# Optimization experiments

Hardware: AMD Instinct MI355X
Metric: run time of the kernel (lower is better)

## Reference

```python
import jax, jax.numpy as jnp
import numpy as np

N = 4096   # in_features
M = 4096   # out_features
RANK, FT_RANK = 128, 64
Q_SCALE, R_SCALE, L_SCALE, GLOBAL_SCALE = 0.9, 1.05, 1.1, 1.0


def fwht(x):
    """Normalized fast Walsh-Hadamard transform over last dim (power of 2).
    Matches matmul_hadU/hadUt for power-of-2 sizes (H symmetric, 1/sqrt(n))."""
    B, n = x.shape
    y, h = x, 1
    while h < n:
        y = y.reshape(B, n // (2 * h), 2, h)
        a, b = y[:, :, 0, :], y[:, :, 1, :]
        y = jnp.stack((a + b, a - b), axis=2)
        h *= 2
    return y.reshape(B, n) * (1.0 / np.sqrt(n)).astype(np.float32)


def dequant(grid, idxs, scale, n_cols):
    # E8P dequant: gather 8-dim lattice vectors, reshape to [rows, n_cols].
    return grid[idxs].reshape(idxs.shape[0], n_cols) * jnp.float32(scale)


def setup_inputs() -> dict:
    key = jax.random.key(0)
    ks = jax.random.split(key, 9)
    return {
        "x": jax.random.normal(ks[0], (4, 2048, N), jnp.float32),
        "SU": jnp.sign(jax.random.normal(ks[1], (N,), jnp.float32)),
        "SV": jnp.sign(jax.random.normal(ks[2], (M,), jnp.float32)),
        "grid": jax.random.normal(ks[3], (65536, 8), jnp.float32) * 0.05,
        "L_ft": jax.random.normal(ks[4], (M, FT_RANK), jnp.float32) * 0.05,
        "R_ft": jax.random.normal(ks[5], (FT_RANK, N), jnp.float32) * 0.05,
        "Q_idxs": jax.random.randint(ks[6], (M, N // 8), 0, 65536, jnp.int32),
        "R_idxs": jax.random.randint(ks[7], (RANK - FT_RANK, N // 8), 0, 65536, jnp.int32),
        "L_idxs": jax.random.randint(ks[8], (RANK - FT_RANK, M // 8), 0, 65536, jnp.int32),
    }


def reference(x, SU, SV, grid, L_ft, R_ft, Q_idxs, R_idxs, L_idxs):
    shape = x.shape
    xf = x.reshape(-1, N) * SU            # [T, n]
    xh = fwht(xf)                          # left randomized Hadamard (hadUt)
    # Q path (x/32 then *scale*32 cancels; applied via scale on W).
    W_q = dequant(grid, Q_idxs, Q_SCALE, N)          # [m, n]
    out = xh @ W_q.T                                  # [T, m]
    # Quantized low-rank path: xR = x @ W_R^T; out += xR @ W_L (transposed L).
    W_r = dequant(grid, R_idxs, R_SCALE, N)           # [r, n]
    W_l = dequant(grid, L_idxs, L_SCALE, M)           # [r, m]
    xR = xh @ W_r.T                                   # [T, r]
    out = out + xR @ W_l                              # [T, m]
    # Fine-tunable LoRA path.
    out = out + (xh @ R_ft.T) @ L_ft.T                # [T, m]
    out = fwht(out)                                   # right Hadamard (hadU)
    out = out * SV * jnp.float32(GLOBAL_SCALE)
    return out.reshape(shape[:-1] + (M,))
```

## Files before the change

kernel.cpp:

```cpp
#include <hip/hip_runtime.h>
#include <stdint.h>
#include <stddef.h>


typedef __attribute__((ext_vector_type(8))) __bf16 bf16x8;
typedef __attribute__((ext_vector_type(4))) float f32x4;

#define DEVFN static __device__ __forceinline__

typedef const __attribute__((address_space(1))) void* as1cvp;
typedef __attribute__((address_space(3))) void* as3vp;

DEVFN void async_g2l16(const void* g, void* l) {
  __builtin_amdgcn_global_load_lds((as1cvp)g, (as3vp)l, 16, 0, 0);
}

DEVFN void fwht16(float* v) {
  #pragma unroll
  for (int h = 1; h < 16; h <<= 1) {
    #pragma unroll
    for (int i = 0; i < 16; ++i) {
      if ((i & h) == 0) {
        float a = v[i], b = v[i + h];
        v[i] = a + b;
        v[i + h] = a - b;
      }
    }
  }
}

DEVFN int padi(int i) { return i + (i >> 4) + (i >> 8); }

template<int MODE>
__global__ __launch_bounds__(256)
void fwht_rows(const float* in, const float* __restrict__ sgn,
               __bf16* __restrict__ outb, float* outf)
{
  __shared__ float s[4366];
  const int row = blockIdx.x;
  const int t = threadIdx.x;
  const float* src = in + (size_t)row * 4096;
  float v[16];

  #pragma unroll
  for (int j4 = 0; j4 < 4; ++j4) {
    f32x4 xv = *(const f32x4*)(src + t * 16 + j4 * 4);
    #pragma unroll
    for (int q = 0; q < 4; ++q) v[j4 * 4 + q] = xv[q];
  }
  if (MODE == 0) {
    #pragma unroll
    for (int j = 0; j < 16; ++j) v[j] *= sgn[t * 16 + j];
  }
  fwht16(v);
  {
    const int base = t * 17 + (t >> 4);
    #pragma unroll
    for (int j = 0; j < 16; ++j) s[base + j] = v[j];
  }
  __syncthreads();

  const int base2 = (t & 15) + ((t >> 4) << 8);
  #pragma unroll
  for (int i = 0; i < 16; ++i) v[i] = s[padi(base2 + (i << 4))];
  fwht16(v);
  #pragma unroll
  for (int i = 0; i < 16; ++i) s[padi(base2 + (i << 4))] = v[i];
  __syncthreads();

  #pragma unroll
  for (int i = 0; i < 16; ++i) v[i] = s[padi(t + (i << 8))];
  fwht16(v);

  if (MODE == 0) {
    #pragma unroll
    for (int i = 0; i < 16; ++i)
      outb[(size_t)row * 4096 + t + (i << 8)] = (__bf16)(v[i] * 0.015625f);
  } else {
    #pragma unroll
    for (int i = 0; i < 16; ++i) {
      int c = t + (i << 8);
      outf[(size_t)row * 4096 + c] = v[i] * 0.015625f * sgn[c];
    }
  }
}

__global__ __launch_bounds__(256)
void prep_uv(const float* __restrict__ grid8,
             const float* __restrict__ Lft, const float* __restrict__ Rft,
             const int* __restrict__ Lidx, const int* __restrict__ Ridx,
             __bf16* __restrict__ Ut, __bf16* __restrict__ Vt)
{
  int tid = blockIdx.x * 256 + threadIdx.x;
  const int half = 4096 * 128;
  bool isV = tid >= half;
  int e = isV ? tid - half : tid;
  int j = e >> 7;
  int r = e & 127;
  float v;
  if (!isV) {
    if (r < 64) v = 1.1f * grid8[(size_t)Lidx[r * 512 + (j >> 3)] * 8 + (j & 7)];
    else        v = Lft[(size_t)j * 64 + (r - 64)];
    Ut[e] = (__bf16)v;
  } else {
    if (r < 64) v = 1.05f * grid8[(size_t)Ridx[r * 512 + (j >> 3)] * 8 + (j & 7)];
    else        v = Rft[(size_t)(r - 64) * 4096 + j];
    Vt[e] = (__bf16)v;
  }
}

template<int K, int EPI>
__global__ __launch_bounds__(256)
void gemm_bt(const __bf16* __restrict__ A, const __bf16* __restrict__ B,
             float* __restrict__ Cf, __bf16* __restrict__ Cb,
             const int* __restrict__ Qidx, const float* __restrict__ grid8,
             int Nn, int nbx)
{
  __shared__ __bf16 sA[128 * 64];
  __shared__ __bf16 sB[128 * 64];

  const int nwg = gridDim.x;
  const int orig = blockIdx.x;
  const int cpx = nwg >> 3;
  const int wg = (orig & 7) * cpx + (orig >> 3);
  const int bm = wg / nbx, bn = wg % nbx;

  const int t = threadIdx.x;
  const int lane = t & 63;
  const int w = t >> 6;
  const int wr = w >> 1, wc = w & 1;

  const int aRow0 = bm * 128;
  const int bRow0 = bn * 128;

  f32x4 acc[4][4] = {};

  #pragma unroll 1
  for (int k0 = 0; k0 < K; k0 += 64) {
    #pragma unroll
    for (int i = 0; i < 4; ++i) {
      int u = i * 256 + t;
      int row = u >> 3, cs = u & 7;
      int c = cs ^ (row & 7);
      async_g2l16(A + (size_t)(aRow0 + row) * K + k0 + c * 8, &sA[u * 8]);
      async_g2l16(B + (size_t)(bRow0 + row) * K + k0 + c * 8, &sB[u * 8]);
    }
    asm volatile("s_waitcnt vmcnt(0)" ::: "memory");
    __syncthreads();

    bf16x8 a[4][2], b[4][2];
    #pragma unroll
    for (int m = 0; m < 4; ++m) {
      #pragma unroll
      for (int kk = 0; kk < 2; ++kk) {
        int c = kk * 4 + (lane >> 4);
        int rowA = wr * 64 + m * 16 + (lane & 15);
        int uA = rowA * 8 + (c ^ (rowA & 7));
        a[m][kk] = *(const bf16x8*)&sA[uA * 8];
        int rowB = wc * 64 + m * 16 + (lane & 15);
        int uB = rowB * 8 + (c ^ (rowB & 7));
        b[m][kk] = *(const bf16x8*)&sB[uB * 8];
      }
    }
    #pragma unroll
    for (int kk = 0; kk < 2; ++kk)
      #pragma unroll
      for (int m = 0; m < 4; ++m)
        #pragma unroll
        for (int n = 0; n < 4; ++n)
          acc[m][n] = __builtin_amdgcn_mfma_f32_16x16x32_bf16(
              a[m][kk], b[n][kk], acc[m][n], 0, 0, 0);
    __syncthreads();
  }

  #pragma unroll
  for (int m = 0; m < 4; ++m) {
    #pragma unroll
    for (int n = 0; n < 4; ++n) {
      int gr = aRow0 + wr * 64 + m * 16 + ((lane >> 4) << 2);
      int gc = bRow0 + wc * 64 + n * 16 + (lane & 15);
      #pragma unroll
      for (int q = 0; q < 4; ++q) {
        float v = acc[m][n][q];
        if constexpr (EPI == 0) {
          Cf[(size_t)(gr + q) * Nn + gc] = v;
        } else {
          int idx = Qidx[(size_t)(gr + q) * (Nn >> 3) + (gc >> 3)];
          v += 0.9f * grid8[(size_t)idx * 8 + (gc & 7)];
          Cb[(size_t)(gr + q) * Nn + gc] = (__bf16)v;
        }
      }
    }
  }
}

extern "C" void kernel_launch(void* const* d_in, const int* in_sizes, int n_in,
                              void* d_out, int out_size, void* d_ws, size_t ws_size,
                              hipStream_t stream) {
  const float* x    = (const float*)d_in[0];
  const float* SU   = (const float*)d_in[1];
  const float* SV   = (const float*)d_in[2];
  const float* grid = (const float*)d_in[3];
  const float* Lft  = (const float*)d_in[4];
  const float* Rft  = (const float*)d_in[5];
  const int*   Qidx = (const int*)d_in[6];
  const int*   Ridx = (const int*)d_in[7];
  const int*   Lidx = (const int*)d_in[8];
  float* out = (float*)d_out;

  char* ws = (char*)d_ws;
  __bf16* xh = (__bf16*)ws;
  __bf16* Wc = (__bf16*)(ws + ((size_t)64 << 20));
  __bf16* Ut = (__bf16*)(ws + ((size_t)96 << 20));
  __bf16* Vt = (__bf16*)(ws + ((size_t)97 << 20));

  prep_uv<<<4096, 256, 0, stream>>>(grid, Lft, Rft, Lidx, Ridx, Ut, Vt);
  fwht_rows<0><<<8192, 256, 0, stream>>>(x, SU, xh, nullptr);
  gemm_bt<128, 1><<<1024, 256, 0, stream>>>(Ut, Vt, nullptr, Wc, Qidx, grid, 4096, 32);
  gemm_bt<4096, 0><<<2048, 256, 0, stream>>>(xh, Wc, out, nullptr, nullptr, nullptr, 4096, 32);
  fwht_rows<1><<<8192, 256, 0, stream>>>(out, SV, nullptr, out);
}
```

Measured before the change: 663.2 us.

## Replace main GEMM with 256x256-tile, 4-stage pipelined kernel; vectorize FWHT I/O

The main 8192x4096x4096 GEMM moves from a 128x128 tile kernel, which loads and waits synchronously every k-step, to a 256x256 tile kernel with 512 threads. The new kernel uses a 4-deep LDS ring buffer prefetching three k-tiles ahead, partial vmcnt waits, and raised priority around the MFMA block. This aims to hide global load latency and cut redundant operand traffic, at the cost of a large LDS footprint and high register pressure per wave. The FWHT kernels also stage results through LDS so they can do contiguous vector stores, and they load the sign vectors with vector loads instead of strided scalar accesses.

```diff
diff --git a/kernel.cpp b/kernel.cpp
--- a/kernel.cpp
+++ b/kernel.cpp
@@ -39,25 +39,30 @@
   __shared__ float s[4366];
   const int row = blockIdx.x;
   const int t = threadIdx.x;
-  const float* src = in + (size_t)row * 4096;
+  const int base1 = t * 17 + (t >> 4);
   float v[16];
 
-  #pragma unroll
-  for (int j4 = 0; j4 < 4; ++j4) {
-    f32x4 xv = *(const f32x4*)(src + t * 16 + j4 * 4);
-    #pragma unroll
-    for (int q = 0; q < 4; ++q) v[j4 * 4 + q] = xv[q];
+  {
+    const float* src = in + (size_t)row * 4096 + t * 16;
+    #pragma unroll
+    for (int j4 = 0; j4 < 4; ++j4) {
+      f32x4 xv = *(const f32x4*)(src + j4 * 4);
+      #pragma unroll
+      for (int q = 0; q < 4; ++q) v[j4 * 4 + q] = xv[q];
+    }
   }
   if (MODE == 0) {
-    #pragma unroll
-    for (int j = 0; j < 16; ++j) v[j] *= sgn[t * 16 + j];
+    const f32x4* sg4 = (const f32x4*)(sgn + t * 16);
+    #pragma unroll
+    for (int j4 = 0; j4 < 4; ++j4) {
+      f32x4 sv = sg4[j4];
+      #pragma unroll
+      for (int q = 0; q < 4; ++q) v[j4 * 4 + q] *= sv[q];
+    }
   }
   fwht16(v);
-  {
-    const int base = t * 17 + (t >> 4);
-    #pragma unroll
-    for (int j = 0; j < 16; ++j) s[base + j] = v[j];
-  }
+  #pragma unroll
+  for (int j = 0; j < 16; ++j) s[base1 + j] = v[j];
   __syncthreads();
 
   const int base2 = (t & 15) + ((t >> 4) << 8);
@@ -71,16 +76,29 @@
   #pragma unroll
   for (int i = 0; i < 16; ++i) v[i] = s[padi(t + (i << 8))];
   fwht16(v);
+  #pragma unroll
+  for (int i = 0; i < 16; ++i) s[padi(t + (i << 8))] = v[i];
+  __syncthreads();
 
   if (MODE == 0) {
-    #pragma unroll
-    for (int i = 0; i < 16; ++i)
-      outb[(size_t)row * 4096 + t + (i << 8)] = (__bf16)(v[i] * 0.015625f);
+    bf16x8 o0, o1;
+    #pragma unroll
+    for (int j = 0; j < 8; ++j) o0[j] = (__bf16)(s[base1 + j] * 0.015625f);
+    #pragma unroll
+    for (int j = 0; j < 8; ++j) o1[j] = (__bf16)(s[base1 + 8 + j] * 0.015625f);
+    __bf16* dst = outb + (size_t)row * 4096 + t * 16;
+    *(bf16x8*)dst = o0;
+    *(bf16x8*)(dst + 8) = o1;
   } else {
-    #pragma unroll
-    for (int i = 0; i < 16; ++i) {
-      int c = t + (i << 8);
-      outf[(size_t)row * 4096 + c] = v[i] * 0.015625f * sgn[c];
+    const f32x4* sg4 = (const f32x4*)(sgn + t * 16);
+    float* dst = outf + (size_t)row * 4096 + t * 16;
+    #pragma unroll
+    for (int j4 = 0; j4 < 4; ++j4) {
+      f32x4 sv = sg4[j4];
+      f32x4 ov;
+      #pragma unroll
+      for (int q = 0; q < 4; ++q) ov[q] = s[base1 + j4 * 4 + q] * 0.015625f * sv[q];
+      *(f32x4*)(dst + j4 * 4) = ov;
     }
   }
 }
@@ -109,10 +127,10 @@
   }
 }
 
-template<int K, int EPI>
+template<int K>
 __global__ __launch_bounds__(256)
 void gemm_bt(const __bf16* __restrict__ A, const __bf16* __restrict__ B,
-             float* __restrict__ Cf, __bf16* __restrict__ Cb,
+             __bf16* __restrict__ Cb,
              const int* __restrict__ Qidx, const float* __restrict__ grid8,
              int Nn, int nbx)
 {
@@ -140,10 +158,10 @@
     #pragma unroll
     for (int i = 0; i < 4; ++i) {
       int u = i * 256 + t;
-      int row = u >> 3, cs = u & 7;
-      int c = cs ^ (row & 7);
-      async_g2l16(A + (size_t)(aRow0 + row) * K + k0 + c * 8, &sA[u * 8]);
-      async_g2l16(B + (size_t)(bRow0 + row) * K + k0 + c * 8, &sB[u * 8]);
+      int rowu = u >> 3, cs = u & 7;
+      int c = cs ^ (rowu & 7);
+      async_g2l16(A + (size_t)(aRow0 + rowu) * K + k0 + c * 8, &sA[u * 8]);
+      async_g2l16(B + (size_t)(bRow0 + rowu) * K + k0 + c * 8, &sB[u * 8]);
     }
     asm volatile("s_waitcnt vmcnt(0)" ::: "memory");
     __syncthreads();
@@ -182,14 +200,118 @@
       #pragma unroll
       for (int q = 0; q < 4; ++q) {
         float v = acc[m][n][q];
-        if constexpr (EPI == 0) {
-          Cf[(size_t)(gr + q) * Nn + gc] = v;
-        } else {
-          int idx = Qidx[(size_t)(gr + q) * (Nn >> 3) + (gc >> 3)];
-          v += 0.9f * grid8[(size_t)idx * 8 + (gc & 7)];
-          Cb[(size_t)(gr + q) * Nn + gc] = (__bf16)v;
-        }
+        int idx = Qidx[(size_t)(gr + q) * (Nn >> 3) + (gc >> 3)];
+        v += 0.9f * grid8[(size_t)idx * 8 + (gc & 7)];
+        Cb[(size_t)(gr + q) * Nn + gc] = (__bf16)v;
       }
+    }
+  }
+}
+
+template<int NT>
+__global__ __launch_bounds__(512, 2)
+void gemm256(const __bf16* __restrict__ A, const __bf16* __restrict__ B,
+             float* __restrict__ Cf, int Nn, int nbx)
+{
+  constexpr int K = NT * 32;
+  __shared__ __bf16 lds[4 * 2 * 8192];
+
+  const int nwg = gridDim.x;
+  const int orig = blockIdx.x;
+  const int cpx = nwg >> 3;
+  const int wg = (orig & 7) * cpx + (orig >> 3);
+  const int bm = wg / nbx, bn = wg % nbx;
+
+  const int tid = threadIdx.x;
+  const int lane = tid & 63;
+  const int wid = tid >> 6;
+  const int wm = wid >> 2;
+  const int wn = wid & 3;
+
+  const int aRow0 = bm * 256;
+  const int bRow0 = bn * 256;
+
+  auto stage = [&](int t) {
+    __bf16* dA = &lds[((t & 3) * 2 + 0) * 8192];
+    __bf16* dB = &lds[((t & 3) * 2 + 1) * 8192];
+    const __bf16* sAg = A + (size_t)aRow0 * K + t * 32;
+    const __bf16* sBg = B + (size_t)bRow0 * K + t * 32;
+    #pragma unroll
+    for (int i = 0; i < 2; ++i) {
+      int u = i * 512 + tid;
+      int prow = u >> 3, slot = u & 7;
+      int chunk = slot ^ (prow & 7);
+      int r = 2 * prow + (chunk >> 2);
+      int k8 = chunk & 3;
+      async_g2l16(sAg + (size_t)r * K + k8 * 8, dA + u * 8);
+    }
+    #pragma unroll
+    for (int i = 0; i < 2; ++i) {
+      int u = i * 512 + tid;
+      int prow = u >> 3, slot = u & 7;
+      int chunk = slot ^ (prow & 7);
+      int r = 2 * prow + (chunk >> 2);
+      int k8 = chunk & 3;
+      async_g2l16(sBg + (size_t)r * K + k8 * 8, dB + u * 8);
+    }
+  };
+
+  const int k8l = lane >> 4;
+  const int rl = lane & 15;
+
+  f32x4 acc[8][4] = {};
+
+  stage(0); stage(1); stage(2);
+  asm volatile("s_waitcnt vmcnt(8)" ::: "memory");
+  __syncthreads();
+
+  #pragma unroll 1
+  for (int t = 0; t < NT; ++t) {
+    if (t + 3 < NT) stage(t + 3);
+
+    const __bf16* bufA = &lds[((t & 3) * 2 + 0) * 8192];
+    const __bf16* bufB = &lds[((t & 3) * 2 + 1) * 8192];
+
+    bf16x8 af[8], bfr[4];
+    #pragma unroll
+    for (int m = 0; m < 8; ++m) {
+      int r = wm * 128 + m * 16 + rl;
+      int prow = r >> 1;
+      int slot = (((r & 1) << 2) | k8l) ^ (prow & 7);
+      af[m] = *(const bf16x8*)(bufA + (prow * 8 + slot) * 8);
+    }
+    #pragma unroll
+    for (int n = 0; n < 4; ++n) {
+      int r = wn * 64 + n * 16 + rl;
+      int prow = r >> 1;
+      int slot = (((r & 1) << 2) | k8l) ^ (prow & 7);
+      bfr[n] = *(const bf16x8*)(bufB + (prow * 8 + slot) * 8);
+    }
+
+    __builtin_amdgcn_s_setprio(1);
+    #pragma unroll
+    for (int m = 0; m < 8; ++m)
+      #pragma unroll
+      for (int n = 0; n < 4; ++n)
+        acc[m][n] = __builtin_amdgcn_mfma_f32_16x16x32_bf16(
+            af[m], bfr[n], acc[m][n], 0, 0, 0);
+    __builtin_amdgcn_s_setprio(0);
+
+    if (t + 3 < NT)      asm volatile("s_waitcnt vmcnt(8)" ::: "memory");
+    else if (t + 2 < NT) asm volatile("s_waitcnt vmcnt(4)" ::: "memory");
+    else if (t + 1 < NT) asm volatile("s_waitcnt vmcnt(0)" ::: "memory");
+    __syncthreads();
+  }
+
+  #pragma unroll
+  for (int m = 0; m < 8; ++m) {
+    #pragma unroll
+    for (int n = 0; n < 4; ++n) {
+      int gr = aRow0 + wm * 128 + m * 16 + ((lane >> 4) << 2);
+      int gc = bRow0 + wn * 64 + n * 16 + (lane & 15);
+      #pragma unroll
+      for (int q = 0; q < 4; ++q)
+        Cf[(size_t)(gr + q) * Nn + gc] = acc[m][n][q];
     }
   }
 }
@@ -216,7 +338,7 @@
 
   prep_uv<<<4096, 256, 0, stream>>>(grid, Lft, Rft, Lidx, Ridx, Ut, Vt);
   fwht_rows<0><<<8192, 256, 0, stream>>>(x, SU, xh, nullptr);
-  gemm_bt<128, 1><<<1024, 256, 0, stream>>>(Ut, Vt, nullptr, Wc, Qidx, grid, 4096, 32);
-  gemm_bt<4096, 0><<<2048, 256, 0, stream>>>(xh, Wc, out, nullptr, nullptr, nullptr, 4096, 32);
+  gemm_bt<128><<<1024, 256, 0, stream>>>(Ut, Vt, Wc, Qidx, grid, 4096, 32);
+  gemm256<128><<<512, 512, 0, stream>>>(xh, Wc, out, 4096, 16);
   fwht_rows<1><<<8192, 256, 0, stream>>>(out, SV, nullptr, out);
 }
```

Measured after the change: 589.6 us. -11.1%, faster.
